# Optimization experiments

Hardware: AMD Instinct MI355X
Metric: run time of the kernel (lower is better)

## Reference

```python
import jax, jax.numpy as jnp
import numpy as np
import math

D_MODEL = 768
NHEAD = 12
D_HEAD = D_MODEL // NHEAD
TAU = 300.0
NEG = -1e9

def setup_inputs() -> dict:
    key = jax.random.key(0)
    ks = jax.random.split(key, 12)
    N, L, D = 64, 512, D_MODEL
    tokens = jax.random.normal(ks[0], (N, L, D), dtype=jnp.float32)
    ts = jax.random.uniform(ks[1], (N, L, 1), dtype=jnp.float32) * 3600.0  # seconds in a 1h window
    mask = jnp.ones((N, L, 1), dtype=jnp.float32)
    s = 1.0 / math.sqrt(D)
    Wq = jax.random.normal(ks[2], (D, D), dtype=jnp.float32) * s
    bq = jnp.zeros((D,), dtype=jnp.float32)
    Wk = jax.random.normal(ks[3], (D, D), dtype=jnp.float32) * s
    bk = jnp.zeros((D,), dtype=jnp.float32)
    Wv = jax.random.normal(ks[4], (D, D), dtype=jnp.float32) * s
    bv = jnp.zeros((D,), dtype=jnp.float32)
    Wo = jax.random.normal(ks[5], (D, D), dtype=jnp.float32) * s
    bo = jnp.zeros((D,), dtype=jnp.float32)
    readout = jax.random.normal(ks[6], (1, 1, D), dtype=jnp.float32)
    return dict(tokens=tokens, ts=ts, mask=mask, Wq=Wq, bq=bq, Wk=Wk, bk=bk,
                Wv=Wv, bv=bv, Wo=Wo, bo=bo, readout=readout)

def _heads(x, N, L):
    return x.reshape(N, L, NHEAD, D_HEAD).transpose(0, 2, 1, 3)  # (N,H,L,dh)

def reference(tokens, ts, mask, Wq, bq, Wk, bk, Wv, bv, Wo, bo, readout):
    N, L, D = tokens.shape
    scale = 1.0 / math.sqrt(D_HEAD)
    # time-decay bias: log(exp(-|dt|/tau) + 1e-12)
    t = (ts - ts[:, :1, :])[..., 0]                       # (N,L)
    dt = jnp.abs(t[:, :, None] - t[:, None, :])           # (N,L,L)
    bias = jnp.log(jnp.exp(-dt / max(TAU, 1e-6)) + 1e-12)
    q = _heads(tokens @ Wq.T + bq, N, L)
    k = _heads(tokens @ Wk.T + bk, N, L)
    v = _heads(tokens @ Wv.T + bv, N, L)
    attn = jnp.einsum('nhqd,nhkd->nhqk', q, k) * scale + bias[:, None, :, :]
    key_pad = mask[..., 0] <= 0                           # (N,L)
    attn = jnp.where(key_pad[:, None, None, :], NEG, attn)
    A = jax.nn.softmax(attn, axis=-1)
    out = jnp.einsum('nhqk,nhkd->nhqd', A, v).transpose(0, 2, 1, 3).reshape(N, L, D)
    out = (out @ Wo.T + bo) * mask
    # readout pooling attention (single learned query)
    qh = jnp.broadcast_to(readout, (N, 1, D)).reshape(N, 1, NHEAD, D_HEAD).transpose(0, 2, 1, 3)
    kh = _heads(out, N, L)
    pool = jnp.einsum('nhqd,nhkd->nhqk', qh, kh) * scale  # (N,H,1,L)
    pool = jnp.where(key_pad[:, None, None, :], NEG, pool)
    P = jax.nn.softmax(pool, axis=-1)
    pooled = jnp.einsum('nhqk,nhkd->nhqd', P, kh).transpose(0, 2, 1, 3).reshape(N, 1, D)
    return pooled[:, 0, :]
```

## Files before the change

kernel.cpp:

```cpp
#include <hip/hip_runtime.h>
#include <stdint.h>

#define AS1 __attribute__((address_space(1)))
#define AS3 __attribute__((address_space(3)))

typedef __bf16 bf16x8 __attribute__((ext_vector_type(8)));
typedef float  f32x4  __attribute__((ext_vector_type(4)));
typedef float  f32x16 __attribute__((ext_vector_type(16)));

#define MFMA16(a, b, c) __builtin_amdgcn_mfma_f32_16x16x32_bf16((a), (b), (c), 0, 0, 0)
#define MFMA32(a, b, c) __builtin_amdgcn_mfma_f32_32x32x16_bf16((a), (b), (c), 0, 0, 0)

#define SEQ   512
#define NBAT  64
#define DM    768
#define NH    12
#define DH    64
#define NQKV  2304
#define NTOK  (NBAT * SEQ)
#define NKB   12

__device__ __forceinline__ uint16_t f2bf(float x) {
  uint32_t u = __float_as_uint(x);
  return (uint16_t)((u + 0x7FFFu + ((u >> 16) & 1u)) >> 16);
}

__device__ __forceinline__ void async16(uint16_t* lds, const uint16_t* g) {
  __builtin_amdgcn_global_load_lds((AS1 void*)(uintptr_t)(const void*)g,
                                   (AS3 void*)lds, 16, 0, 0);
}

__device__ __forceinline__ int swz(int r) { return (r ^ (r >> 3)) & 7; }

__global__ __launch_bounds__(256) void k_cvt(
    const float* __restrict__ tokens,
    const float* __restrict__ Wq, const float* __restrict__ Wk,
    const float* __restrict__ Wv, const float* __restrict__ Wo,
    const float* __restrict__ bq, const float* __restrict__ bk, const float* __restrict__ bv,
    uint16_t* __restrict__ X, uint16_t* __restrict__ Wqkv_pk, uint16_t* __restrict__ Wob_pk,
    float* __restrict__ bqkv) {
  int i = blockIdx.x * 256 + threadIdx.x;
  {
    const float4* sp = (const float4*)tokens;
    float4 a = sp[2 * i], b = sp[2 * i + 1];
    union { uint16_t u[8]; uint4 v; } o;
    o.u[0] = f2bf(a.x); o.u[1] = f2bf(a.y); o.u[2] = f2bf(a.z); o.u[3] = f2bf(a.w);
    o.u[4] = f2bf(b.x); o.u[5] = f2bf(b.y); o.u[6] = f2bf(b.z); o.u[7] = f2bf(b.w);
    ((uint4*)X)[i] = o.v;
  }
  if (i < 221184) {
    int lane = i & 63, ks = (i >> 6) & 3, kb = (i >> 8) % NKB, g = i / 3072;
    int row = g * 32 + (lane & 31);
    int k   = kb * 64 + ks * 16 + (lane >> 5) * 8;
    const float* src = (row < 768)  ? Wq + (size_t)row * 768 + k
                     : (row < 1536) ? Wk + (size_t)(row - 768) * 768 + k
                                    : Wv + (size_t)(row - 1536) * 768 + k;
    float4 a = *(const float4*)src, b = *(const float4*)(src + 4);
    union { uint16_t u[8]; uint4 v; } o;
    o.u[0] = f2bf(a.x); o.u[1] = f2bf(a.y); o.u[2] = f2bf(a.z); o.u[3] = f2bf(a.w);
    o.u[4] = f2bf(b.x); o.u[5] = f2bf(b.y); o.u[6] = f2bf(b.z); o.u[7] = f2bf(b.w);
    ((uint4*)Wqkv_pk)[i] = o.v;
  }
  if (i < 73728) {
    int lane = i & 63, ks = (i >> 6) & 3, kb = (i >> 8) % NKB, g = i / 3072;
    int row = g * 32 + (lane & 31);
    int k   = kb * 64 + ks * 16 + (lane >> 5) * 8;
    const float* src = Wo + (size_t)row * 768 + k;
    float4 a = *(const float4*)src, b = *(const float4*)(src + 4);
    union { uint16_t u[8]; uint4 v; } o;
    o.u[0] = f2bf(a.x); o.u[1] = f2bf(a.y); o.u[2] = f2bf(a.z); o.u[3] = f2bf(a.w);
    o.u[4] = f2bf(b.x); o.u[5] = f2bf(b.y); o.u[6] = f2bf(b.z); o.u[7] = f2bf(b.w);
    ((uint4*)Wob_pk)[i] = o.v;
  }
  if (i < 768) { bqkv[i] = bq[i]; bqkv[i + 768] = bk[i]; bqkv[i + 1536] = bv[i]; }
}

__global__ __launch_bounds__(256) void k_gemm_bt(
    const uint16_t* __restrict__ A, const uint16_t* __restrict__ Bpk,
    const float* __restrict__ bias, const float* __restrict__ rowscale,
    uint16_t* __restrict__ C, int ldc, int ncol) {
  __shared__ uint16_t Alds[128 * 64];
  const int tid  = threadIdx.x;
  const int w    = tid >> 6, lane = tid & 63;
  const int wu   = __builtin_amdgcn_readfirstlane(w);
  const int l32  = lane & 31, kh = lane >> 5;
  const int sup  = blockIdx.x / (32 * ncol);
  const int t    = blockIdx.x % (32 * ncol);
  const int row0 = (sup * 32 + (t & 31)) * 128, col0 = (t >> 5) * 128;
  const int wrow = (w >> 1) * 64,   wcol = (w & 1) * 64;

  const uint16_t* bw = Bpk + (size_t)((col0 >> 5) + (w & 1) * 2) * (NKB * 2048) + lane * 8;

  f32x16 acc[2][2] = {};
  for (int kb = 0; kb < NKB; ++kb) {
    bf16x8 bfr[4][2];
#pragma unroll
    for (int ks = 0; ks < 4; ++ks)
#pragma unroll
      for (int nt = 0; nt < 2; ++nt)
        bfr[ks][nt] = *(const bf16x8*)(bw + (size_t)nt * (NKB * 2048) + (kb * 4 + ks) * 512);
    __syncthreads();
#pragma unroll
    for (int j = 0; j < 4; ++j) {
      int cid = j * 256 + w * 64 + lane;
      int r = cid >> 3, cc = cid & 7, c = cc ^ swz(r);
      async16(&Alds[(j * 256 + wu * 64) * 8],
              A + (size_t)(row0 + r) * 768 + kb * 64 + c * 8);
    }
    __syncthreads();
#pragma unroll
    for (int ks = 0; ks < 4; ++ks) {
      bf16x8 af[2];
#pragma unroll
      for (int mt = 0; mt < 2; ++mt) {
        int r = wrow + mt * 32 + l32;
        int c = (ks * 2 + kh) ^ swz(r);
        af[mt] = *(const bf16x8*)&Alds[r * 64 + c * 8];
      }
#pragma unroll
      for (int mt = 0; mt < 2; ++mt)
#pragma unroll
        for (int nt = 0; nt < 2; ++nt)
          acc[mt][nt] = MFMA32(af[mt], bfr[ks][nt], acc[mt][nt]);
    }
  }
#pragma unroll
  for (int nt = 0; nt < 2; ++nt) {
    int col = col0 + wcol + nt * 32 + l32;
    float bv = bias[col];
#pragma unroll
    for (int mt = 0; mt < 2; ++mt) {
#pragma unroll
      for (int rg = 0; rg < 16; ++rg) {
        int row = row0 + wrow + mt * 32 + (rg & 3) + 8 * (rg >> 2) + 4 * kh;
        float v = acc[mt][nt][rg] + bv;
        if (rowscale) v *= rowscale[row];
        C[(size_t)row * ldc + col] = f2bf(v);
      }
    }
  }
}

__global__ __launch_bounds__(256) void k_attn(
    const uint16_t* __restrict__ QKV, const float* __restrict__ ts,
    const float* __restrict__ mask, uint16_t* __restrict__ Aout) {
  __shared__ uint16_t Klds[64 * 64];
  __shared__ uint16_t Vt[64 * 72];
  __shared__ uint16_t Plds[4][32 * 72];
  __shared__ float tkl[SEQ];

  const int tid = threadIdx.x, w = tid >> 6, lane = tid & 63;
  const int wu = __builtin_amdgcn_readfirstlane(w);
  const int quad = lane >> 4, l16 = lane & 15;
  int b = blockIdx.x;
  int xcd = b & 7, i = b >> 3;
  int qt = i & 3;
  int hg = xcd * 96 + (i >> 2);
  int n = hg / NH, h = hg % NH;
  const int q0 = qt * 128 + w * 32;
  const size_t rowbase = (size_t)n * SEQ * NQKV;

  const float c1 = 0.125f * 1.44269504f;
  const float c2 = 1.44269504f / 300.0f;

  for (int l = tid; l < SEQ; l += 256) {
    float t = ts[n * SEQ + l] * c2;
    tkl[l] = (mask[n * SEQ + l] > 0.f) ? t : 3e38f;
  }

  bf16x8 qf[2][2];
  float tq[2][4];
#pragma unroll
  for (int qs = 0; qs < 2; ++qs) {
    int qr = q0 + qs * 16 + l16;
    const uint16_t* qp = QKV + rowbase + (size_t)qr * NQKV + h * DH;
#pragma unroll
    for (int dsp = 0; dsp < 2; ++dsp)
      qf[qs][dsp] = *(const bf16x8*)(qp + dsp * 32 + quad * 8);
#pragma unroll
    for (int rg = 0; rg < 4; ++rg)
      tq[qs][rg] = ts[n * SEQ + q0 + qs * 16 + quad * 4 + rg] * c2;
  }

  f32x4 accO[2][4] = {};
  f32x4 accL[2] = {};
  bf16x8 ones_b;
  {
    union { uint16_t u[8]; bf16x8 v; } t;
    uint16_t o = (l16 == 0) ? 0x3F80 : 0;
#pragma unroll
    for (int j = 0; j < 8; ++j) t.u[j] = o;
    ones_b = t.v;
  }
  uint16_t* Pw = &Plds[w][0];

  for (int k0 = 0; k0 < SEQ; k0 += 64) {
    __syncthreads();
#pragma unroll
    for (int j = 0; j < 2; ++j) {
      int cid = j * 256 + w * 64 + lane;
      int r = cid >> 3, cc = cid & 7, c = cc ^ swz(r);
      const uint16_t* g = QKV + rowbase + (size_t)(k0 + r) * NQKV + DM + h * DH + c * 8;
      async16(&Klds[(j * 256 + wu * 64) * 8], g);
    }
    {
      int r = tid & 63, db = (tid >> 6) * 16;
      const uint16_t* g = QKV + rowbase + (size_t)(k0 + r) * NQKV + 2 * DM + h * DH + db;
      union { uint4 v; uint16_t u[8]; } a0, a1;
      a0.v = *(const uint4*)g;
      a1.v = *(const uint4*)(g + 8);
#pragma unroll
      for (int j = 0; j < 8; ++j) Vt[(db + j) * 72 + r] = a0.u[j];
#pragma unroll
      for (int j = 0; j < 8; ++j) Vt[(db + 8 + j) * 72 + r] = a1.u[j];
    }
    __syncthreads();

#pragma unroll
    for (int kt = 0; kt < 2; ++kt) {
      f32x4 s[2][2] = {};
#pragma unroll
      for (int dsp = 0; dsp < 2; ++dsp) {
        bf16x8 kf[2];
#pragma unroll
        for (int ksu = 0; ksu < 2; ++ksu) {
          int r = kt * 32 + 2 * l16 + ksu;
          int c = (dsp * 4 + quad) ^ swz(r);
          kf[ksu] = *(const bf16x8*)&Klds[r * 64 + c * 8];
        }
#pragma unroll
        for (int qs = 0; qs < 2; ++qs)
#pragma unroll
          for (int ksu = 0; ksu < 2; ++ksu)
            s[qs][ksu] = MFMA16(qf[qs][dsp], kf[ksu], s[qs][ksu]);
      }
      float tk0 = tkl[k0 + kt * 32 + 2 * l16];
      float tk1 = tkl[k0 + kt * 32 + 2 * l16 + 1];
#pragma unroll
      for (int qs = 0; qs < 2; ++qs) {
#pragma unroll
        for (int rg = 0; rg < 4; ++rg) {
          float d0 = fabsf(tq[qs][rg] - tk0);
          float d1 = fabsf(tq[qs][rg] - tk1);
          float p0 = __builtin_amdgcn_exp2f(fmaf(s[qs][0][rg], c1, -d0));
          float p1 = __builtin_amdgcn_exp2f(fmaf(s[qs][1][rg], c1, -d1));
          uint32_t u = (__float_as_uint(p0) >> 16) | (__float_as_uint(p1) & 0xFFFF0000u);
          *(uint32_t*)(Pw + (qs * 16 + quad * 4 + rg) * 72 + kt * 32 + 2 * l16) = u;
        }
      }
      bf16x8 vb[4];
#pragma unroll
      for (int dt = 0; dt < 4; ++dt)
        vb[dt] = *(const bf16x8*)&Vt[(dt * 16 + l16) * 72 + kt * 32 + quad * 8];
#pragma unroll
      for (int qs = 0; qs < 2; ++qs) {
        bf16x8 pa = *(const bf16x8*)(Pw + (qs * 16 + l16) * 72 + kt * 32 + quad * 8);
#pragma unroll
        for (int dt = 0; dt < 4; ++dt)
          accO[qs][dt] = MFMA16(pa, vb[dt], accO[qs][dt]);
        accL[qs] = MFMA16(pa, ones_b, accL[qs]);
      }
    }
  }
#pragma unroll
  for (int qs = 0; qs < 2; ++qs) {
    float inv[4];
#pragma unroll
    for (int rg = 0; rg < 4; ++rg) {
      float lv = __shfl(accL[qs][rg], lane & 48, 64);
      inv[rg] = 1.0f / lv;
    }
#pragma unroll
    for (int dt = 0; dt < 4; ++dt) {
#pragma unroll
      for (int rg = 0; rg < 4; ++rg) {
        int qr = q0 + qs * 16 + quad * 4 + rg;
        float v = accO[qs][dt][rg] * inv[rg];
        Aout[(size_t)(n * SEQ + qr) * DM + h * DH + dt * 16 + l16] = f2bf(v);
      }
    }
  }
}

__global__ __launch_bounds__(256) void k_pool(
    const uint16_t* __restrict__ Out, const float* __restrict__ mask,
    const float* __restrict__ readout, float* __restrict__ dst) {
  __shared__ float rsl[64];
  __shared__ float ex[SEQ];
  __shared__ float red[4];
  __shared__ float part[8][64];
  int b = blockIdx.x;
  int n = b / NH, h = b % NH;
  int tid = threadIdx.x;
  if (tid < 64) rsl[tid] = readout[h * DH + tid];
  __syncthreads();

  float suml = 0.f;
  for (int l = tid; l < SEQ; l += 256) {
    const uint16_t* rowp = Out + (size_t)(n * SEQ + l) * DM + h * DH;
    float acc = 0.f;
#pragma unroll
    for (int c = 0; c < 8; ++c) {
      union { uint4 v; uint16_t u[8]; } t;
      t.v = *(const uint4*)(rowp + c * 8);
#pragma unroll
      for (int j = 0; j < 8; ++j)
        acc += __uint_as_float(((uint32_t)t.u[j]) << 16) * rsl[c * 8 + j];
    }
    float e = __builtin_amdgcn_exp2f(acc * (0.125f * 1.44269504f));
    e = (mask[n * SEQ + l] > 0.f) ? e : 0.f;
    ex[l] = e;
    suml += e;
  }
#pragma unroll
  for (int off = 32; off; off >>= 1) suml += __shfl_down(suml, off, 64);
  if ((tid & 63) == 0) red[tid >> 6] = suml;
  __syncthreads();
  float inv = 1.0f / (red[0] + red[1] + red[2] + red[3]);

  int d0 = (tid & 31) * 2, ch = tid >> 5;
  float a0 = 0.f, a1 = 0.f;
  for (int l = ch * 64; l < ch * 64 + 64; ++l) {
    uint32_t pv = *(const uint32_t*)(Out + (size_t)(n * SEQ + l) * DM + h * DH + d0);
    float e = ex[l];
    a0 = fmaf(__uint_as_float(pv << 16), e, a0);
    a1 = fmaf(__uint_as_float(pv & 0xFFFF0000u), e, a1);
  }
  part[ch][d0] = a0;
  part[ch][d0 + 1] = a1;
  __syncthreads();
  if (tid < 64) {
    float s = 0.f;
#pragma unroll
    for (int c = 0; c < 8; ++c) s += part[c][tid];
    dst[n * DM + h * DH + tid] = s * inv;
  }
}

extern "C" void kernel_launch(void* const* d_in, const int* in_sizes, int n_in,
                              void* d_out, int out_size, void* d_ws, size_t ws_size,
                              hipStream_t stream) {
  const float* tokens  = (const float*)d_in[0];
  const float* ts      = (const float*)d_in[1];
  const float* mask    = (const float*)d_in[2];
  const float* Wq      = (const float*)d_in[3];
  const float* bq      = (const float*)d_in[4];
  const float* Wk      = (const float*)d_in[5];
  const float* bk      = (const float*)d_in[6];
  const float* Wv      = (const float*)d_in[7];
  const float* bv      = (const float*)d_in[8];
  const float* Wo      = (const float*)d_in[9];
  const float* bo      = (const float*)d_in[10];
  const float* readout = (const float*)d_in[11];

  char* ws = (char*)d_ws;
  uint16_t* X    = (uint16_t*)ws;
  uint16_t* Wqkv = (uint16_t*)(ws + 50331648);
  uint16_t* Wob  = (uint16_t*)(ws + 53870592);
  float*    bqkv = (float*)   (ws + 55050240);
  uint16_t* QKV  = (uint16_t*)(ws + 55059456);
  uint16_t* attn = X;
  uint16_t* Outb = QKV;

  k_cvt<<<12288, 256, 0, stream>>>(tokens, Wq, Wk, Wv, Wo, bq, bk, bv, X, Wqkv, Wob, bqkv);
  k_gemm_bt<<<4608, 256, 0, stream>>>(X, Wqkv, bqkv, nullptr, QKV, NQKV, 18);
  k_attn<<<3072, 256, 0, stream>>>(QKV, ts, mask, attn);
  k_gemm_bt<<<1536, 256, 0, stream>>>(attn, Wob, bo, mask, Outb, DM, 6);
  k_pool<<<768, 256, 0, stream>>>(Outb, mask, readout, (float*)d_out);
}
```

Measured before the change: 501.6 us.

## Replace projection GEMM with 256x256 tiled, 8-wave, LDS-pipelined MFMA16 kernel

Replaces the 128x128-tile GEMM, which read B from pre-packed global fragments and reloaded A into LDS with two barriers per k-step, with a 256x256-tile, 512-thread kernel. Both A and B are staged through swizzled LDS with async global-to-LDS loads, double-buffered across k-steps, and interleaved with four MFMA16 quadrants per step using s_setprio and explicit waitcnt and barrier scheduling. Weights are now stored row-major instead of pre-packed, and block indices are remapped so tiles are spread across the XCDs. The larger tiles raise data reuse but cut the block count, so the second GEMM gets only 384 blocks, and the 64 KB of LDS per block limits occupancy.

```diff
diff --git a/kernel.cpp b/kernel.cpp
--- a/kernel.cpp
+++ b/kernel.cpp
@@ -6,10 +6,8 @@
 
 typedef __bf16 bf16x8 __attribute__((ext_vector_type(8)));
 typedef float  f32x4  __attribute__((ext_vector_type(4)));
-typedef float  f32x16 __attribute__((ext_vector_type(16)));
 
 #define MFMA16(a, b, c) __builtin_amdgcn_mfma_f32_16x16x32_bf16((a), (b), (c), 0, 0, 0)
-#define MFMA32(a, b, c) __builtin_amdgcn_mfma_f32_32x32x16_bf16((a), (b), (c), 0, 0, 0)
 
 #define SEQ   512
 #define NBAT  64
@@ -37,7 +35,7 @@
     const float* __restrict__ Wq, const float* __restrict__ Wk,
     const float* __restrict__ Wv, const float* __restrict__ Wo,
     const float* __restrict__ bq, const float* __restrict__ bk, const float* __restrict__ bv,
-    uint16_t* __restrict__ X, uint16_t* __restrict__ Wqkv_pk, uint16_t* __restrict__ Wob_pk,
+    uint16_t* __restrict__ X, uint16_t* __restrict__ Wqkv, uint16_t* __restrict__ Wob,
     float* __restrict__ bqkv) {
   int i = blockIdx.x * 256 + threadIdx.x;
   {
@@ -49,9 +47,7 @@
     ((uint4*)X)[i] = o.v;
   }
   if (i < 221184) {
-    int lane = i & 63, ks = (i >> 6) & 3, kb = (i >> 8) % NKB, g = i / 3072;
-    int row = g * 32 + (lane & 31);
-    int k   = kb * 64 + ks * 16 + (lane >> 5) * 8;
+    int row = i / 96, k = (i % 96) * 8;
     const float* src = (row < 768)  ? Wq + (size_t)row * 768 + k
                      : (row < 1536) ? Wk + (size_t)(row - 768) * 768 + k
                                     : Wv + (size_t)(row - 1536) * 768 + k;
@@ -59,86 +55,184 @@
     union { uint16_t u[8]; uint4 v; } o;
     o.u[0] = f2bf(a.x); o.u[1] = f2bf(a.y); o.u[2] = f2bf(a.z); o.u[3] = f2bf(a.w);
     o.u[4] = f2bf(b.x); o.u[5] = f2bf(b.y); o.u[6] = f2bf(b.z); o.u[7] = f2bf(b.w);
-    ((uint4*)Wqkv_pk)[i] = o.v;
+    ((uint4*)Wqkv)[i] = o.v;
   }
   if (i < 73728) {
-    int lane = i & 63, ks = (i >> 6) & 3, kb = (i >> 8) % NKB, g = i / 3072;
-    int row = g * 32 + (lane & 31);
-    int k   = kb * 64 + ks * 16 + (lane >> 5) * 8;
+    int row = i / 96, k = (i % 96) * 8;
     const float* src = Wo + (size_t)row * 768 + k;
     float4 a = *(const float4*)src, b = *(const float4*)(src + 4);
     union { uint16_t u[8]; uint4 v; } o;
     o.u[0] = f2bf(a.x); o.u[1] = f2bf(a.y); o.u[2] = f2bf(a.z); o.u[3] = f2bf(a.w);
     o.u[4] = f2bf(b.x); o.u[5] = f2bf(b.y); o.u[6] = f2bf(b.z); o.u[7] = f2bf(b.w);
-    ((uint4*)Wob_pk)[i] = o.v;
+    ((uint4*)Wob)[i] = o.v;
   }
   if (i < 768) { bqkv[i] = bq[i]; bqkv[i + 768] = bk[i]; bqkv[i + 1536] = bv[i]; }
 }
 
-__global__ __launch_bounds__(256) void k_gemm_bt(
-    const uint16_t* __restrict__ A, const uint16_t* __restrict__ Bpk,
+__global__ __launch_bounds__(512, 2) void k_gemm8(
+    const uint16_t* __restrict__ A, const uint16_t* __restrict__ B,
     const float* __restrict__ bias, const float* __restrict__ rowscale,
     uint16_t* __restrict__ C, int ldc, int ncol) {
-  __shared__ uint16_t Alds[128 * 64];
-  const int tid  = threadIdx.x;
-  const int w    = tid >> 6, lane = tid & 63;
-  const int wu   = __builtin_amdgcn_readfirstlane(w);
-  const int l32  = lane & 31, kh = lane >> 5;
-  const int sup  = blockIdx.x / (32 * ncol);
-  const int t    = blockIdx.x % (32 * ncol);
-  const int row0 = (sup * 32 + (t & 31)) * 128, col0 = (t >> 5) * 128;
-  const int wrow = (w >> 1) * 64,   wcol = (w & 1) * 64;
-
-  const uint16_t* bw = Bpk + (size_t)((col0 >> 5) + (w & 1) * 2) * (NKB * 2048) + lane * 8;
-
-  f32x16 acc[2][2] = {};
-  for (int kb = 0; kb < NKB; ++kb) {
-    bf16x8 bfr[4][2];
-#pragma unroll
-    for (int ks = 0; ks < 4; ++ks)
-#pragma unroll
-      for (int nt = 0; nt < 2; ++nt)
-        bfr[ks][nt] = *(const bf16x8*)(bw + (size_t)nt * (NKB * 2048) + (kb * 4 + ks) * 512);
-    __syncthreads();
-#pragma unroll
-    for (int j = 0; j < 4; ++j) {
-      int cid = j * 256 + w * 64 + lane;
-      int r = cid >> 3, cc = cid & 7, c = cc ^ swz(r);
-      async16(&Alds[(j * 256 + wu * 64) * 8],
-              A + (size_t)(row0 + r) * 768 + kb * 64 + c * 8);
-    }
-    __syncthreads();
-#pragma unroll
-    for (int ks = 0; ks < 4; ++ks) {
-      bf16x8 af[2];
-#pragma unroll
-      for (int mt = 0; mt < 2; ++mt) {
-        int r = wrow + mt * 32 + l32;
-        int c = (ks * 2 + kh) ^ swz(r);
-        af[mt] = *(const bf16x8*)&Alds[r * 64 + c * 8];
-      }
-#pragma unroll
-      for (int mt = 0; mt < 2; ++mt)
-#pragma unroll
-        for (int nt = 0; nt < 2; ++nt)
-          acc[mt][nt] = MFMA32(af[mt], bfr[ks][nt], acc[mt][nt]);
-    }
-  }
-#pragma unroll
-  for (int nt = 0; nt < 2; ++nt) {
-    int col = col0 + wcol + nt * 32 + l32;
-    float bv = bias[col];
-#pragma unroll
-    for (int mt = 0; mt < 2; ++mt) {
-#pragma unroll
-      for (int rg = 0; rg < 16; ++rg) {
-        int row = row0 + wrow + mt * 32 + (rg & 3) + 8 * (rg >> 2) + 4 * kh;
-        float v = acc[mt][nt][rg] + bv;
-        if (rowscale) v *= rowscale[row];
-        C[(size_t)row * ldc + col] = f2bf(v);
-      }
-    }
-  }
+  __shared__ __align__(16) uint16_t lds[8 * 8192];
+  const int tid = threadIdx.x;
+  const int w = tid >> 6, lane = tid & 63;
+  const int wu = __builtin_amdgcn_readfirstlane(w);
+  const int wm = w >> 2, wn = w & 3;
+  const int l16 = lane & 15, quad = lane >> 4;
+
+  const int cpx = gridDim.x >> 3;
+  const int t = (blockIdx.x & 7) * cpx + (blockIdx.x >> 3);
+  const int rowt = t / ncol, colt = t - rowt * ncol;
+  const int row0 = rowt << 8, col0 = colt << 8;
+
+  const int r0s = tid >> 3, c0s = (tid & 7) ^ swz(r0s);
+  const int r1s = 64 + r0s, c1s = (tid & 7) ^ swz(r1s);
+
+  const int rA = wm * 64 + l16;
+  const int rB = wn * 32 + l16;
+
+#define STAGE(mat, rbase, kt, slot_) do {                                      \
+    async16(&lds[(slot_) * 8192 + wu * 512],                                   \
+            (mat) + (size_t)((rbase) + r0s) * 768 + (kt) * 64 + c0s * 8);      \
+    async16(&lds[(slot_) * 8192 + 4096 + wu * 512],                            \
+            (mat) + (size_t)((rbase) + r1s) * 768 + (kt) * 64 + c1s * 8);      \
+  } while (0)
+
+  f32x4 acc[2][4][2][2] = {};
+  bf16x8 a0[4][2], a1[4][2], b0[2][2], b1[2][2];
+
+  STAGE(A, row0,       0, 0);
+  STAGE(A, row0 + 128, 0, 1);
+  STAGE(B, col0,       0, 2);
+  STAGE(B, col0 + 128, 0, 3);
+  STAGE(A, row0,       1, 4);
+  STAGE(B, col0,       1, 6);
+  STAGE(B, col0 + 128, 1, 7);
+  asm volatile("s_waitcnt vmcnt(6)" ::: "memory");
+  __builtin_amdgcn_s_barrier();
+  asm volatile("" ::: "memory");
+
+#pragma unroll 2
+  for (int W = 0; W < NKB; ++W) {
+    const int p = (W & 1) << 2, q = p ^ 4;
+#pragma unroll
+    for (int mf = 0; mf < 4; ++mf) {
+      int r = rA + mf * 16;
+#pragma unroll
+      for (int kf = 0; kf < 2; ++kf) {
+        int c = (kf * 4 + quad) ^ swz(r);
+        a0[mf][kf] = *(const bf16x8*)&lds[(p + 0) * 8192 + r * 64 + c * 8];
+      }
+    }
+#pragma unroll
+    for (int nf = 0; nf < 2; ++nf) {
+      int r = rB + nf * 16;
+#pragma unroll
+      for (int kf = 0; kf < 2; ++kf) {
+        int c = (kf * 4 + quad) ^ swz(r);
+        b0[nf][kf] = *(const bf16x8*)&lds[(p + 2) * 8192 + r * 64 + c * 8];
+      }
+    }
+    if (W + 1 < NKB) STAGE(A, row0 + 128, W + 1, q + 1);
+    __builtin_amdgcn_s_barrier();
+    asm volatile("s_waitcnt lgkmcnt(0)" ::: "memory");
+    __builtin_amdgcn_sched_barrier(0);
+    __builtin_amdgcn_s_setprio(1);
+#pragma unroll
+    for (int mf = 0; mf < 4; ++mf)
+#pragma unroll
+      for (int nf = 0; nf < 2; ++nf)
+#pragma unroll
+        for (int kf = 0; kf < 2; ++kf)
+          acc[0][mf][0][nf] = MFMA16(a0[mf][kf], b0[nf][kf], acc[0][mf][0][nf]);
+    __builtin_amdgcn_s_setprio(0);
+    __builtin_amdgcn_s_barrier();
+    asm volatile("" ::: "memory");
+#pragma unroll
+    for (int nf = 0; nf < 2; ++nf) {
+      int r = rB + nf * 16;
+#pragma unroll
+      for (int kf = 0; kf < 2; ++kf) {
+        int c = (kf * 4 + quad) ^ swz(r);
+        b1[nf][kf] = *(const bf16x8*)&lds[(p + 3) * 8192 + r * 64 + c * 8];
+      }
+    }
+    if (W + 2 < NKB) STAGE(A, row0, W + 2, p + 0);
+    __builtin_amdgcn_s_barrier();
+    asm volatile("s_waitcnt lgkmcnt(0)" ::: "memory");
+    __builtin_amdgcn_sched_barrier(0);
+    __builtin_amdgcn_s_setprio(1);
+#pragma unroll
+    for (int mf = 0; mf < 4; ++mf)
+#pragma unroll
+      for (int nf = 0; nf < 2; ++nf)
+#pragma unroll
+        for (int kf = 0; kf < 2; ++kf)
+          acc[0][mf][1][nf] = MFMA16(a0[mf][kf], b1[nf][kf], acc[0][mf][1][nf]);
+    __builtin_amdgcn_s_setprio(0);
+    __builtin_amdgcn_s_barrier();
+    asm volatile("" ::: "memory");
+#pragma unroll
+    for (int mf = 0; mf < 4; ++mf) {
+      int r = rA + mf * 16;
+#pragma unroll
+      for (int kf = 0; kf < 2; ++kf) {
+        int c = (kf * 4 + quad) ^ swz(r);
+        a1[mf][kf] = *(const bf16x8*)&lds[(p + 1) * 8192 + r * 64 + c * 8];
+      }
+    }
+    if (W + 2 < NKB) STAGE(B, col0, W + 2, p + 2);
+    __builtin_amdgcn_s_barrier();
+    asm volatile("s_waitcnt lgkmcnt(0)" ::: "memory");
+    __builtin_amdgcn_sched_barrier(0);
+    __builtin_amdgcn_s_setprio(1);
+#pragma unroll
+    for (int mf = 0; mf < 4; ++mf)
+#pragma unroll
+      for (int nf = 0; nf < 2; ++nf)
+#pragma unroll
+        for (int kf = 0; kf < 2; ++kf)
+          acc[1][mf][1][nf] = MFMA16(a1[mf][kf], b1[nf][kf], acc[1][mf][1][nf]);
+    __builtin_amdgcn_s_setprio(0);
+    __builtin_amdgcn_s_barrier();
+    asm volatile("" ::: "memory");
+    if (W + 2 < NKB) STAGE(B, col0 + 128, W + 2, p + 3);
+    if (W < NKB - 2) asm volatile("s_waitcnt vmcnt(6)" ::: "memory");
+    else             asm volatile("s_waitcnt vmcnt(0)" ::: "memory");
+    __builtin_amdgcn_s_barrier();
+    __builtin_amdgcn_sched_barrier(0);
+    __builtin_amdgcn_s_setprio(1);
+#pragma unroll
+    for (int mf = 0; mf < 4; ++mf)
+#pragma unroll
+      for (int nf = 0; nf < 2; ++nf)
+#pragma unroll
+        for (int kf = 0; kf < 2; ++kf)
+          acc[1][mf][0][nf] = MFMA16(a1[mf][kf], b0[nf][kf], acc[1][mf][0][nf]);
+    __builtin_amdgcn_s_setprio(0);
+    __builtin_amdgcn_s_barrier();
+    asm volatile("" ::: "memory");
+  }
+#undef STAGE
+
+#pragma unroll
+  for (int nh = 0; nh < 2; ++nh)
+#pragma unroll
+    for (int nf = 0; nf < 2; ++nf) {
+      int col = col0 + nh * 128 + wn * 32 + nf * 16 + l16;
+      float bv = bias[col];
+#pragma unroll
+      for (int mh = 0; mh < 2; ++mh)
+#pragma unroll
+        for (int mf = 0; mf < 4; ++mf)
+#pragma unroll
+          for (int rg = 0; rg < 4; ++rg) {
+            int row = row0 + mh * 128 + wm * 64 + mf * 16 + quad * 4 + rg;
+            float v = acc[mh][mf][nh][nf][rg] + bv;
+            if (rowscale) v *= rowscale[row];
+            C[(size_t)row * ldc + col] = f2bf(v);
+          }
+    }
 }
 
 __global__ __launch_bounds__(256) void k_attn(
@@ -363,8 +457,8 @@
   uint16_t* Outb = QKV;
 
   k_cvt<<<12288, 256, 0, stream>>>(tokens, Wq, Wk, Wv, Wo, bq, bk, bv, X, Wqkv, Wob, bqkv);
-  k_gemm_bt<<<4608, 256, 0, stream>>>(X, Wqkv, bqkv, nullptr, QKV, NQKV, 18);
+  k_gemm8<<<1152, 512, 0, stream>>>(X, Wqkv, bqkv, nullptr, QKV, NQKV, 9);
   k_attn<<<3072, 256, 0, stream>>>(QKV, ts, mask, attn);
-  k_gemm_bt<<<1536, 256, 0, stream>>>(attn, Wob, bo, mask, Outb, DM, 6);
+  k_gemm8<<<384, 512, 0, stream>>>(attn, Wob, bo, mask, Outb, DM, 3);
   k_pool<<<768, 256, 0, stream>>>(Outb, mask, readout, (float*)d_out);
 }
```

After: 542.8 us. 1.08x slower.

## Remap GEMM blocks per XCD and vectorize V transpose stores into LDS

Applied to the files above, without the earlier changes.

The GEMM block index is remapped so that each of the 8 XCDs (blockIdx mod 8) handles a contiguous band of row tiles, with the column tiles for a 16-row group scheduled together. This is meant to improve L2 reuse of A and B tiles within each XCD. In the attention kernel, the V transpose now loads a 4x4 tile per thread and writes 8-byte vector stores into LDS instead of 16 scalar 2-byte stores, which cuts LDS store instructions. The remapping assumes the grid divides evenly by 8*ncol and by 16.

```diff
diff --git a/kernel.cpp b/kernel.cpp
--- a/kernel.cpp
+++ b/kernel.cpp
@@ -84,9 +84,12 @@
   const int w    = tid >> 6, lane = tid & 63;
   const int wu   = __builtin_amdgcn_readfirstlane(w);
   const int l32  = lane & 31, kh = lane >> 5;
-  const int sup  = blockIdx.x / (32 * ncol);
-  const int t    = blockIdx.x % (32 * ncol);
-  const int row0 = (sup * 32 + (t & 31)) * 128, col0 = (t >> 5) * 128;
+  const int xcd  = blockIdx.x & 7, bi = blockIdx.x >> 3;
+  const int span = 16 * ncol;
+  const int rg   = bi / span, jj = bi - rg * span;
+  const int rpx  = (int)(gridDim.x >> 3) / ncol;
+  const int rt   = xcd * rpx + rg * 16 + (jj & 15);
+  const int row0 = rt * 128, col0 = (jj >> 4) * 128;
   const int wrow = (w >> 1) * 64,   wcol = (w & 1) * 64;
 
   const uint16_t* bw = Bpk + (size_t)((col0 >> 5) + (w & 1) * 2) * (NKB * 2048) + lane * 8;
@@ -131,9 +134,9 @@
 #pragma unroll
     for (int mt = 0; mt < 2; ++mt) {
 #pragma unroll
-      for (int rg = 0; rg < 16; ++rg) {
-        int row = row0 + wrow + mt * 32 + (rg & 3) + 8 * (rg >> 2) + 4 * kh;
-        float v = acc[mt][nt][rg] + bv;
+      for (int rg2 = 0; rg2 < 16; ++rg2) {
+        int row = row0 + wrow + mt * 32 + (rg2 & 3) + 8 * (rg2 >> 2) + 4 * kh;
+        float v = acc[mt][nt][rg2] + bv;
         if (rowscale) v *= rowscale[row];
         C[(size_t)row * ldc + col] = f2bf(v);
       }
@@ -204,15 +207,19 @@
       async16(&Klds[(j * 256 + wu * 64) * 8], g);
     }
     {
-      int r = tid & 63, db = (tid >> 6) * 16;
-      const uint16_t* g = QKV + rowbase + (size_t)(k0 + r) * NQKV + 2 * DM + h * DH + db;
-      union { uint4 v; uint16_t u[8]; } a0, a1;
-      a0.v = *(const uint4*)g;
-      a1.v = *(const uint4*)(g + 8);
-#pragma unroll
-      for (int j = 0; j < 8; ++j) Vt[(db + j) * 72 + r] = a0.u[j];
-#pragma unroll
-      for (int j = 0; j < 8; ++j) Vt[(db + 8 + j) * 72 + r] = a1.u[j];
+      int r0v = (tid & 15) * 4, db = (tid >> 4) * 4;
+      const uint16_t* g = QKV + rowbase + (size_t)(k0 + r0v) * NQKV + 2 * DM + h * DH + db;
+      union { uint16_t u[4]; uint2 d; } v0, v1, v2, v3;
+      v0.d = *(const uint2*)g;
+      v1.d = *(const uint2*)(g + NQKV);
+      v2.d = *(const uint2*)(g + 2 * NQKV);
+      v3.d = *(const uint2*)(g + 3 * NQKV);
+#pragma unroll
+      for (int j = 0; j < 4; ++j) {
+        union { uint16_t u[4]; uint2 d; } wv;
+        wv.u[0] = v0.u[j]; wv.u[1] = v1.u[j]; wv.u[2] = v2.u[j]; wv.u[3] = v3.u[j];
+        *(uint2*)&Vt[(db + j) * 72 + r0v] = wv.d;
+      }
     }
     __syncthreads();
 
```

After: 525.2 us. +4.7%, slower.

## Prefetch next V tile into registers and double-buffer P in attention loop

Applied to the files above, without the earlier changes.

Restructures the attention key loop so the next block's V rows are loaded into registers while the current block computes, then written to LDS after a barrier along with issuing the next K async load. The P scratch buffer is split per kt half with a narrower stride. s_setprio and sched_barriers are added around the MFMA sections. The aim is to hide global-load latency for V behind compute. The cost is extra registers, and K still loads only after compute, so its latency is not overlapped.

```diff
diff --git a/kernel.cpp b/kernel.cpp
--- a/kernel.cpp
+++ b/kernel.cpp
@@ -146,7 +146,7 @@
     const float* __restrict__ mask, uint16_t* __restrict__ Aout) {
   __shared__ uint16_t Klds[64 * 64];
   __shared__ uint16_t Vt[64 * 72];
-  __shared__ uint16_t Plds[4][32 * 72];
+  __shared__ uint16_t Plds[4][2 * 32 * 40];
   __shared__ float tkl[SEQ];
 
   const int tid = threadIdx.x, w = tid >> 6, lane = tid & 63;
@@ -194,31 +194,42 @@
   }
   uint16_t* Pw = &Plds[w][0];
 
-  for (int k0 = 0; k0 < SEQ; k0 += 64) {
-    __syncthreads();
-#pragma unroll
-    for (int j = 0; j < 2; ++j) {
-      int cid = j * 256 + w * 64 + lane;
-      int r = cid >> 3, cc = cid & 7, c = cc ^ swz(r);
-      const uint16_t* g = QKV + rowbase + (size_t)(k0 + r) * NQKV + DM + h * DH + c * 8;
-      async16(&Klds[(j * 256 + wu * 64) * 8], g);
-    }
-    {
-      int r = tid & 63, db = (tid >> 6) * 16;
-      const uint16_t* g = QKV + rowbase + (size_t)(k0 + r) * NQKV + 2 * DM + h * DH + db;
-      union { uint4 v; uint16_t u[8]; } a0, a1;
-      a0.v = *(const uint4*)g;
-      a1.v = *(const uint4*)(g + 8);
-#pragma unroll
-      for (int j = 0; j < 8; ++j) Vt[(db + j) * 72 + r] = a0.u[j];
-#pragma unroll
-      for (int j = 0; j < 8; ++j) Vt[(db + 8 + j) * 72 + r] = a1.u[j];
-    }
-    __syncthreads();
+  const uint16_t* Kbase = QKV + rowbase + DM + h * DH;
+  const uint16_t* Vbase = QKV + rowbase + 2 * DM + h * DH;
+  const int vr = tid & 63, vdb = (tid >> 6) * 16;
+  uint4 vreg0, vreg1;
+
+#pragma unroll
+  for (int j = 0; j < 2; ++j) {
+    int cid = j * 256 + w * 64 + lane;
+    int r = cid >> 3, cc = cid & 7, c = cc ^ swz(r);
+    async16(&Klds[(j * 256 + wu * 64) * 8], Kbase + (size_t)r * NQKV + c * 8);
+  }
+  vreg0 = *(const uint4*)(Vbase + (size_t)vr * NQKV + vdb);
+  vreg1 = *(const uint4*)(Vbase + (size_t)vr * NQKV + vdb + 8);
+  __syncthreads();
+  {
+    union { uint4 v; uint16_t u[8]; } a0, a1;
+    a0.v = vreg0; a1.v = vreg1;
+#pragma unroll
+    for (int j = 0; j < 8; ++j) Vt[(vdb + j) * 72 + vr] = a0.u[j];
+#pragma unroll
+    for (int j = 0; j < 8; ++j) Vt[(vdb + 8 + j) * 72 + vr] = a1.u[j];
+  }
+  __syncthreads();
+
+  for (int it = 0; it < 8; ++it) {
+    const int k0 = it * 64;
+    if (it < 7) {
+      vreg0 = *(const uint4*)(Vbase + (size_t)(k0 + 64 + vr) * NQKV + vdb);
+      vreg1 = *(const uint4*)(Vbase + (size_t)(k0 + 64 + vr) * NQKV + vdb + 8);
+    }
 
 #pragma unroll
     for (int kt = 0; kt < 2; ++kt) {
+      uint16_t* Pk = Pw + kt * 1280;
       f32x4 s[2][2] = {};
+      __builtin_amdgcn_s_setprio(1);
 #pragma unroll
       for (int dsp = 0; dsp < 2; ++dsp) {
         bf16x8 kf[2];
@@ -234,6 +245,7 @@
           for (int ksu = 0; ksu < 2; ++ksu)
             s[qs][ksu] = MFMA16(qf[qs][dsp], kf[ksu], s[qs][ksu]);
       }
+      __builtin_amdgcn_s_setprio(0);
       float tk0 = tkl[k0 + kt * 32 + 2 * l16];
       float tk1 = tkl[k0 + kt * 32 + 2 * l16 + 1];
 #pragma unroll
@@ -245,22 +257,48 @@
           float p0 = __builtin_amdgcn_exp2f(fmaf(s[qs][0][rg], c1, -d0));
           float p1 = __builtin_amdgcn_exp2f(fmaf(s[qs][1][rg], c1, -d1));
           uint32_t u = (__float_as_uint(p0) >> 16) | (__float_as_uint(p1) & 0xFFFF0000u);
-          *(uint32_t*)(Pw + (qs * 16 + quad * 4 + rg) * 72 + kt * 32 + 2 * l16) = u;
+          *(uint32_t*)(Pk + (qs * 16 + quad * 4 + rg) * 40 + 2 * l16) = u;
         }
       }
+      asm volatile("" ::: "memory");
+      __builtin_amdgcn_sched_barrier(0);
       bf16x8 vb[4];
 #pragma unroll
       for (int dt = 0; dt < 4; ++dt)
         vb[dt] = *(const bf16x8*)&Vt[(dt * 16 + l16) * 72 + kt * 32 + quad * 8];
+      __builtin_amdgcn_s_setprio(1);
 #pragma unroll
       for (int qs = 0; qs < 2; ++qs) {
-        bf16x8 pa = *(const bf16x8*)(Pw + (qs * 16 + l16) * 72 + kt * 32 + quad * 8);
+        bf16x8 pa = *(const bf16x8*)(Pk + (qs * 16 + l16) * 40 + quad * 8);
 #pragma unroll
         for (int dt = 0; dt < 4; ++dt)
           accO[qs][dt] = MFMA16(pa, vb[dt], accO[qs][dt]);
         accL[qs] = MFMA16(pa, ones_b, accL[qs]);
       }
-    }
+      __builtin_amdgcn_s_setprio(0);
+      asm volatile("" ::: "memory");
+      __builtin_amdgcn_sched_barrier(0);
+    }
+
+    __syncthreads();
+    if (it < 7) {
+      {
+        union { uint4 v; uint16_t u[8]; } a0, a1;
+        a0.v = vreg0; a1.v = vreg1;
+#pragma unroll
+        for (int j = 0; j < 8; ++j) Vt[(vdb + j) * 72 + vr] = a0.u[j];
+#pragma unroll
+        for (int j = 0; j < 8; ++j) Vt[(vdb + 8 + j) * 72 + vr] = a1.u[j];
+      }
+#pragma unroll
+      for (int j = 0; j < 2; ++j) {
+        int cid = j * 256 + w * 64 + lane;
+        int r = cid >> 3, cc = cid & 7, c = cc ^ swz(r);
+        async16(&Klds[(j * 256 + wu * 64) * 8],
+                Kbase + (size_t)(k0 + 64 + r) * NQKV + c * 8);
+      }
+    }
+    __syncthreads();
   }
 #pragma unroll
   for (int qs = 0; qs < 2; ++qs) {
```

Result: faster. 488.2 us (-2.7%).
